# Kernel optimization log

Measured on AMD Instinct MI355X. Metric: run time of the kernel, lower is better.

## Reference

```python
import jax, jax.numpy as jnp
import numpy as np

WIDTH = 1.0  # radial_width
AMPLITUDE = (WIDTH ** 0.5) * 1.772637204826652  # ~sqrt(pi*width)
BN_EPS = 1e-3  # keras BatchNormalization default


def sine_pos_encoding(seq_len, hidden, dtype):
    # keras_nlp.layers.SinePositionEncoding, max_wavelength=10000
    position = jnp.arange(seq_len, dtype=dtype)
    min_freq = jnp.asarray(1.0 / 10000.0, dtype)
    timescales = min_freq ** (2 * (jnp.arange(hidden) // 2).astype(dtype) / hidden)
    angles = position[:, None] * timescales[None, :]  # [T, H]
    odd = (jnp.arange(hidden) % 2).astype(dtype)
    return jnp.sin(angles) * (1 - odd) + jnp.cos(angles) * odd


def setup_inputs() -> dict:
    key = jax.random.key(0)
    ks = jax.random.split(key, 4)
    B, T, C, F, K, L = 16, 4096, 8, 64, 11, 4096
    x = jax.random.normal(ks[0], (B, T, C), jnp.float32)
    conv_w = jax.random.normal(ks[1], (K, C, F), jnp.float32) * 0.1
    conv_b = jnp.zeros((F,), jnp.float32)
    gamma = jnp.ones((F,), jnp.float32)
    beta = jnp.zeros((F,), jnp.float32)
    mean = jnp.zeros((F,), jnp.float32)
    var = jnp.ones((F,), jnp.float32)
    # HeNormal init for dense
    dense_w = jax.random.normal(ks[2], (F, L), jnp.float32) * (2.0 / F) ** 0.5
    dense_b = jnp.zeros((L,), jnp.float32)
    return dict(x=x, conv_w=conv_w, conv_b=conv_b, gamma=gamma, beta=beta,
                mean=mean, var=var, dense_w=dense_w, dense_b=dense_b)


def reference(x, conv_w, conv_b, gamma, beta, mean, var, dense_w, dense_b):
    B, T, C = x.shape
    F = conv_w.shape[-1]
    L = dense_w.shape[-1]
    # Conv1D same padding -> [B, T, F]
    h = jax.lax.conv_general_dilated(x, conv_w, (1,), 'SAME',
                                     dimension_numbers=('NWC', 'WIO', 'NWC')) + conv_b
    # BatchNorm (inference form)
    h = (h - mean) / jnp.sqrt(var + BN_EPS) * gamma + beta
    # Softmax over time axis
    h = jax.nn.softmax(h, axis=1)
    # sine positional encoding added
    h = h + sine_pos_encoding(T, F, x.dtype)
    # Dense with sigmoid, rescale to [-1, 1]
    d = jax.nn.sigmoid(h @ dense_w + dense_b) * 2.0 - 1.0  # [B, T, L]
    # ReductionLayer: sum over time -> shift weights [B, L]
    shift = jnp.sum(d, axis=1)
    # ShiftingLayer: Gaussian RBF warp matrix then matmul
    idx_in = jnp.arange(1, T + 1, dtype=x.dtype)                       # [T]
    scale = jnp.asarray(T / L, x.dtype)
    idx_sh = (jnp.arange(1, L + 1, dtype=x.dtype) + shift) * scale     # [B, L]
    M = idx_in[None, None, :] - idx_sh[:, :, None]                     # [B, L, T]
    M = jnp.exp(-(M * M) / WIDTH) / AMPLITUDE
    return jnp.matmul(M, x)  # [B, L, C]
```

## Files before the change

kernel.cpp:

```cpp
#include <hip/hip_runtime.h>
#include <stdint.h>

#define BB 16
#define TT 4096
#define CC 8
#define FF 64
#define KW 11
#define LL 4096

#define L2E 1.442695040888963f
#define NCONV (BB * (TT / 64))

typedef __attribute__((ext_vector_type(8))) short short8;
typedef __attribute__((ext_vector_type(16))) float floatx16;

__device__ float e_buf[(size_t)BB * TT * FF];

__device__ __forceinline__ unsigned short f2b(float f) {
    union { float f; uint32_t i; } v; v.f = f;
    uint32_t x = v.i;
    return (unsigned short)((x + 0x7fffu + ((x >> 16) & 1u)) >> 16);
}
__device__ __forceinline__ float b2f(unsigned short u) {
    union { uint32_t i; float f; } v; v.i = ((uint32_t)u) << 16; return v.f;
}

#define DOT8(acc, ra, rb, wp) \
    acc = fmaf(ra.x, (wp)[0], acc); acc = fmaf(ra.y, (wp)[1], acc); \
    acc = fmaf(ra.z, (wp)[2], acc); acc = fmaf(ra.w, (wp)[3], acc); \
    acc = fmaf(rb.x, (wp)[4], acc); acc = fmaf(rb.y, (wp)[5], acc); \
    acc = fmaf(rb.z, (wp)[6], acc); acc = fmaf(rb.w, (wp)[7], acc);

__global__ __launch_bounds__(256) void k_convsplit(
        const float* __restrict__ x, const float* __restrict__ cw,
        const float* __restrict__ cb, const float* __restrict__ gm,
        const float* __restrict__ bt, const float* __restrict__ mn,
        const float* __restrict__ vr, const float* __restrict__ dw,
        unsigned short* __restrict__ Wt, float* __restrict__ sumexp) {
    if (blockIdx.x >= NCONV) {
        const int idx  = (blockIdx.x - NCONV) * 256 + threadIdx.x;
        const int j    = idx & 7;
        const int ln   = (idx >> 3) & 31;
        const int half = (idx >> 8) & 1;
        const int kf   = (idx >> 9) & 3;
        const int lt   = idx >> 11;
        const int l = lt * 32 + ln;
        const int k = kf * 16 + half * 8 + j;
        const float v = dw[(size_t)k * LL + l];
        const unsigned short hi = f2b(v);
        const unsigned short lo = f2b(v - b2f(hi));
        Wt[idx] = hi;
        Wt[262144 + idx] = lo;
        return;
    }
    __shared__ __align__(16) float xsm[(64 + KW - 1) * CC];
    __shared__ float red[4 * FF];
    const int tid = threadIdx.x;
    const int b  = blockIdx.x / (TT / 64);
    const int t0 = (blockIdx.x % (TT / 64)) * 64;
    const int f = tid & 63, ts = tid >> 6;

    float wreg[KW * CC];
#pragma unroll
    for (int kc = 0; kc < KW * CC; ++kc) wreg[kc] = cw[kc * FF + f];

    for (int i = tid; i < (64 + KW - 1) * CC; i += 256) {
        int row = i >> 3, c = i & 7;
        int t = t0 - (KW / 2) + row;
        xsm[i] = (t >= 0 && t < TT) ? x[((size_t)b * TT + t) * CC + c] : 0.0f;
    }
    const float s  = gm[f] * rsqrtf(vr[f] + 1e-3f);
    const float bb = bt[f] + (cb[f] - mn[f]) * s;
    const float s2 = s * L2E, b2 = bb * L2E;
    __syncthreads();

    float* eb = e_buf + ((size_t)b * TT + t0) * FF + f;
    const float4* xv = (const float4*)xsm;
    float esum = 0.f;
#pragma unroll 1
    for (int c = 0; c < 4; ++c) {
        const int tb = c * 16 + ts * 4;
        float a0 = 0.f, a1 = 0.f, a2 = 0.f, a3 = 0.f;
#pragma unroll
        for (int k = 0; k < KW + 3; ++k) {
            const float4 ra = xv[(tb + k) * 2];
            const float4 rb = xv[(tb + k) * 2 + 1];
            if (k <= 10)           { DOT8(a0, ra, rb, wreg + k * 8); }
            if (k >= 1 && k <= 11) { DOT8(a1, ra, rb, wreg + (k - 1) * 8); }
            if (k >= 2 && k <= 12) { DOT8(a2, ra, rb, wreg + (k - 2) * 8); }
            if (k >= 3)            { DOT8(a3, ra, rb, wreg + (k - 3) * 8); }
        }
        float e0 = __builtin_amdgcn_exp2f(fmaf(a0, s2, b2));
        float e1 = __builtin_amdgcn_exp2f(fmaf(a1, s2, b2));
        float e2 = __builtin_amdgcn_exp2f(fmaf(a2, s2, b2));
        float e3 = __builtin_amdgcn_exp2f(fmaf(a3, s2, b2));
        eb[(tb + 0) * FF] = e0;
        eb[(tb + 1) * FF] = e1;
        eb[(tb + 2) * FF] = e2;
        eb[(tb + 3) * FF] = e3;
        esum += (e0 + e1) + (e2 + e3);
    }
    red[ts * FF + f] = esum;
    __syncthreads();
    if (ts == 0) {
        float tot = red[f] + red[FF + f] + red[2 * FF + f] + red[3 * FF + f];
        atomicAdd(&sumexp[b * FF + f], tot);
    }
}

__global__ __launch_bounds__(512) void k_main(
        const unsigned short* __restrict__ Wt,
        const float* __restrict__ db,  const float* __restrict__ sumexp,
        float* __restrict__ shiftsum) {
    __shared__ __align__(16) unsigned short As[16384];

    const int tid = threadIdx.x;
    const int b  = blockIdx.y;
    const int t0 = blockIdx.x * 128;
    const int f = tid & 63, tq = tid >> 6;

    const float inv_se = 1.0f / sumexp[b * FF + f];
    const float tsf = exp2f(-0.20762050586796017f * (float)(f & ~1));
    const int kfh = ((f >> 4) << 1) | ((f >> 3) & 1);
    const int jj  = f & 7;
    const float ang0 = (float)(t0 + tq) * tsf;
    const float dA = 8.0f * tsf;
    float sv = sinf(ang0), cv = cosf(ang0);
    const float sd = sinf(dA), cd = cosf(dA);

    const float* eb = e_buf + ((size_t)b * TT + t0) * FF + f;
#pragma unroll 4
    for (int i = 0; i < 16; ++i) {
        const int tt = tq + 8 * i;
        float ev = eb[tt * FF];
        float p = (f & 1) ? cv : sv;
        float h = fmaf(ev, inv_se, p);
        const unsigned short hi = f2b(h);
        const unsigned short lo = f2b(h - b2f(hi));
        const int off = ((tt >> 5) * 8 + kfh) * 256 + (tt & 31) * 8 + jj;
        As[off] = hi;
        As[8192 + off] = lo;
        float ns = fmaf(sv, cd, cv * sd);
        float nc = fmaf(cv, cd, -(sv * sd));
        sv = ns; cv = nc;
    }
    __syncthreads();

    const int lane = tid & 63;
    const int wv   = tid >> 6;
    const int half = lane >> 5;
    const int ln31 = lane & 31;
    const int vbase = (half << 9) | (ln31 << 4);
    const char* Ab = (const char*)As;
    const char* Wb = (const char*)Wt;

#pragma unroll 1
    for (int i = 0; i < 16; ++i) {
        const int lt = (i + 2 * wv) & 15;
        const int ltile = lt * 8 + wv;
        const int lbase = ltile * 32;
        const char* wp = Wb + ((size_t)ltile << 12) + vbase;
        short8 Whi[4], Wlo[4];
#pragma unroll
        for (int kf = 0; kf < 4; ++kf) {
            Whi[kf] = *reinterpret_cast<const short8*>(wp + kf * 1024);
            Wlo[kf] = *reinterpret_cast<const short8*>(wp + 524288 + kf * 1024);
        }
        const float dbn = db[lbase + ln31] * (-L2E);

        float ss[4] = {0.f, 0.f, 0.f, 0.f};
#pragma unroll 1
        for (int nt = 0; nt < 4; ++nt) {
            const char* ap = Ab + (nt << 12) + vbase;
            floatx16 acc1 = {0.f, 0.f, 0.f, 0.f, 0.f, 0.f, 0.f, 0.f,
                             0.f, 0.f, 0.f, 0.f, 0.f, 0.f, 0.f, 0.f};
            floatx16 acc2 = acc1;
            __builtin_amdgcn_s_setprio(1);
            {
                short8 Ahi = *reinterpret_cast<const short8*>(ap);
                short8 Alo = *reinterpret_cast<const short8*>(ap + 16384);
                acc1 = __builtin_amdgcn_mfma_f32_32x32x16_bf16(Ahi, Whi[0], acc1, 0, 0, 0);
                acc1 = __builtin_amdgcn_mfma_f32_32x32x16_bf16(Alo, Whi[0], acc1, 0, 0, 0);
                acc1 = __builtin_amdgcn_mfma_f32_32x32x16_bf16(Ahi, Wlo[0], acc1, 0, 0, 0);
                Ahi = *reinterpret_cast<const short8*>(ap + 2048);
                Alo = *reinterpret_cast<const short8*>(ap + 16384 + 2048);
                acc2 = __builtin_amdgcn_mfma_f32_32x32x16_bf16(Ahi, Whi[2], acc2, 0, 0, 0);
                acc2 = __builtin_amdgcn_mfma_f32_32x32x16_bf16(Alo, Whi[2], acc2, 0, 0, 0);
                acc2 = __builtin_amdgcn_mfma_f32_32x32x16_bf16(Ahi, Wlo[2], acc2, 0, 0, 0);
                Ahi = *reinterpret_cast<const short8*>(ap + 1024);
                Alo = *reinterpret_cast<const short8*>(ap + 16384 + 1024);
                acc1 = __builtin_amdgcn_mfma_f32_32x32x16_bf16(Ahi, Whi[1], acc1, 0, 0, 0);
                acc1 = __builtin_amdgcn_mfma_f32_32x32x16_bf16(Alo, Whi[1], acc1, 0, 0, 0);
                acc1 = __builtin_amdgcn_mfma_f32_32x32x16_bf16(Ahi, Wlo[1], acc1, 0, 0, 0);
                Ahi = *reinterpret_cast<const short8*>(ap + 3072);
                Alo = *reinterpret_cast<const short8*>(ap + 16384 + 3072);
                acc2 = __builtin_amdgcn_mfma_f32_32x32x16_bf16(Ahi, Whi[3], acc2, 0, 0, 0);
                acc2 = __builtin_amdgcn_mfma_f32_32x32x16_bf16(Alo, Whi[3], acc2, 0, 0, 0);
                acc2 = __builtin_amdgcn_mfma_f32_32x32x16_bf16(Ahi, Wlo[3], acc2, 0, 0, 0);
            }
            __builtin_amdgcn_s_setprio(0);
#pragma unroll
            for (int q = 0; q < 4; ++q) {
                float e0 = __builtin_amdgcn_exp2f(fmaf(acc1[4 * q + 0], -L2E,
                                                  fmaf(acc2[4 * q + 0], -L2E, dbn)));
                float e1 = __builtin_amdgcn_exp2f(fmaf(acc1[4 * q + 1], -L2E,
                                                  fmaf(acc2[4 * q + 1], -L2E, dbn)));
                float e2 = __builtin_amdgcn_exp2f(fmaf(acc1[4 * q + 2], -L2E,
                                                  fmaf(acc2[4 * q + 2], -L2E, dbn)));
                float e3 = __builtin_amdgcn_exp2f(fmaf(acc1[4 * q + 3], -L2E,
                                                  fmaf(acc2[4 * q + 3], -L2E, dbn)));
                float a0 = 1.f + e0, a1 = 1.f + e1, a2 = 1.f + e2, a3 = 1.f + e3;
                float p01 = a0 * a1, p23 = a2 * a3;
                float num = fmaf(a0 + a1, p23, (a2 + a3) * p01);
                ss[q] = fmaf(num, __builtin_amdgcn_rcpf(p01 * p23), ss[q]);
            }
        }
        float ssum = (ss[0] + ss[1]) + (ss[2] + ss[3]);
        ssum += __shfl_xor(ssum, 32);
        if (half == 0)
            atomicAdd(shiftsum + (size_t)b * LL + lbase + ln31, ssum);
    }
}

__global__ __launch_bounds__(256) void k_warp(
        const float* __restrict__ shiftsum, const float* __restrict__ x,
        float* __restrict__ out) {
    const int idx = blockIdx.x * 256 + threadIdx.x;
    const int l = idx & (LL - 1);
    const int b = idx >> 12;
    const float sh = fmaf(2.0f, shiftsum[idx], -(float)TT);
    const float scale = (float)TT / (float)LL;
    const float center = ((float)(l + 1) + sh) * scale;
    const float R = 7.0f;
    int tlo = (int)ceilf(center - 1.0f - R);
    int thi = (int)floorf(center - 1.0f + R);
    if (tlo < 0) tlo = 0;
    if (thi > TT - 1) thi = TT - 1;
    float acc[CC];
#pragma unroll
    for (int c = 0; c < CC; ++c) acc[c] = 0.f;
    const float inv_amp = (float)(1.0 / 1.772637204826652);
    for (int t = tlo; t <= thi; ++t) {
        float d = (float)(t + 1) - center;
        float w = __expf(-d * d) * inv_amp;
        const float4 x0 = *reinterpret_cast<const float4*>(x + ((size_t)b * TT + t) * CC);
        const float4 x1 = *reinterpret_cast<const float4*>(x + ((size_t)b * TT + t) * CC + 4);
        acc[0] = fmaf(w, x0.x, acc[0]);
        acc[1] = fmaf(w, x0.y, acc[1]);
        acc[2] = fmaf(w, x0.z, acc[2]);
        acc[3] = fmaf(w, x0.w, acc[3]);
        acc[4] = fmaf(w, x1.x, acc[4]);
        acc[5] = fmaf(w, x1.y, acc[5]);
        acc[6] = fmaf(w, x1.z, acc[6]);
        acc[7] = fmaf(w, x1.w, acc[7]);
    }
    float* o = out + (size_t)idx * CC;
    *reinterpret_cast<float4*>(o)     = make_float4(acc[0], acc[1], acc[2], acc[3]);
    *reinterpret_cast<float4*>(o + 4) = make_float4(acc[4], acc[5], acc[6], acc[7]);
}

extern "C" void kernel_launch(void* const* d_in, const int* in_sizes, int n_in,
                              void* d_out, int out_size, void* d_ws, size_t ws_size,
                              hipStream_t stream) {
    const float* x  = (const float*)d_in[0];
    const float* cw = (const float*)d_in[1];
    const float* cb = (const float*)d_in[2];
    const float* gm = (const float*)d_in[3];
    const float* bt = (const float*)d_in[4];
    const float* mn = (const float*)d_in[5];
    const float* vr = (const float*)d_in[6];
    const float* dw = (const float*)d_in[7];
    const float* db = (const float*)d_in[8];

    float* sumexp      = (float*)d_ws;
    float* shiftsum    = sumexp + BB * FF;
    unsigned short* Wt = (unsigned short*)(shiftsum + BB * LL);

    hipMemsetAsync(sumexp, 0, (size_t)(BB * FF + BB * LL) * sizeof(float), stream);

    k_convsplit<<<NCONV + (FF * LL) / 256, 256, 0, stream>>>(
        x, cw, cb, gm, bt, mn, vr, dw, Wt, sumexp);
    k_main<<<dim3(TT / 128, BB), 512, 0, stream>>>(Wt, db, sumexp, shiftsum);
    k_warp<<<(BB * LL) / 256, 256, 0, stream>>>(shiftsum, x, (float*)d_out);
}
```

Baseline: 210.4 us.

## Replace atomics and memset with partial-sum buffers; fold sigmoid scale into MFMA

Float atomics into sumexp and shiftsum are replaced by per-block partial buffers that the consumer kernels reduce, and the hipMemsetAsync is dropped. The dense weights are pre-scaled by -log2(e) and the accumulator is seeded with the scaled bias, so the exp2 takes the MFMA output directly. This also merges the two accumulators into one fully unrolled chain. The cost is serial MFMA dependencies, extra partial-buffer reads in k_main and k_warp, and a different float summation order.

New measurement: 190.3 us. 9.5% less time.

```diff
diff --git a/kernel.cpp b/kernel.cpp
--- a/kernel.cpp
+++ b/kernel.cpp
@@ -15,6 +15,8 @@
 typedef __attribute__((ext_vector_type(16))) float floatx16;
 
 __device__ float e_buf[(size_t)BB * TT * FF];
+__device__ float sumpart[NCONV * FF];
+__device__ float shift_part[(size_t)BB * 32 * LL];
 
 __device__ __forceinline__ unsigned short f2b(float f) {
     union { float f; uint32_t i; } v; v.f = f;
@@ -36,7 +38,7 @@
         const float* __restrict__ cb, const float* __restrict__ gm,
         const float* __restrict__ bt, const float* __restrict__ mn,
         const float* __restrict__ vr, const float* __restrict__ dw,
-        unsigned short* __restrict__ Wt, float* __restrict__ sumexp) {
+        unsigned short* __restrict__ Wt) {
     if (blockIdx.x >= NCONV) {
         const int idx  = (blockIdx.x - NCONV) * 256 + threadIdx.x;
         const int j    = idx & 7;
@@ -46,7 +48,7 @@
         const int lt   = idx >> 11;
         const int l = lt * 32 + ln;
         const int k = kf * 16 + half * 8 + j;
-        const float v = dw[(size_t)k * LL + l];
+        const float v = dw[(size_t)k * LL + l] * (-L2E);
         const unsigned short hi = f2b(v);
         const unsigned short lo = f2b(v - b2f(hi));
         Wt[idx] = hi;
@@ -102,16 +104,13 @@
     }
     red[ts * FF + f] = esum;
     __syncthreads();
-    if (ts == 0) {
-        float tot = red[f] + red[FF + f] + red[2 * FF + f] + red[3 * FF + f];
-        atomicAdd(&sumexp[b * FF + f], tot);
-    }
+    if (ts == 0)
+        sumpart[blockIdx.x * FF + f] = red[f] + red[FF + f] + red[2 * FF + f] + red[3 * FF + f];
 }
 
 __global__ __launch_bounds__(512) void k_main(
         const unsigned short* __restrict__ Wt,
-        const float* __restrict__ db,  const float* __restrict__ sumexp,
-        float* __restrict__ shiftsum) {
+        const float* __restrict__ db, float* __restrict__ dummy) {
     __shared__ __align__(16) unsigned short As[16384];
 
     const int tid = threadIdx.x;
@@ -119,7 +118,12 @@
     const int t0 = blockIdx.x * 128;
     const int f = tid & 63, tq = tid >> 6;
 
-    const float inv_se = 1.0f / sumexp[b * FF + f];
+    float se = 0.f;
+    const float* sp = sumpart + (size_t)b * 64 * FF + f;
+#pragma unroll 8
+    for (int j = 0; j < 64; ++j) se += sp[j * FF];
+    const float inv_se = 1.0f / se;
+
     const float tsf = exp2f(-0.20762050586796017f * (float)(f & ~1));
     const int kfh = ((f >> 4) << 1) | ((f >> 3) & 1);
     const int jj  = f & 7;
@@ -169,46 +173,28 @@
         const float dbn = db[lbase + ln31] * (-L2E);
 
         float ss[4] = {0.f, 0.f, 0.f, 0.f};
-#pragma unroll 1
+#pragma unroll
         for (int nt = 0; nt < 4; ++nt) {
-            const char* ap = Ab + (nt << 12) + vbase;
-            floatx16 acc1 = {0.f, 0.f, 0.f, 0.f, 0.f, 0.f, 0.f, 0.f,
-                             0.f, 0.f, 0.f, 0.f, 0.f, 0.f, 0.f, 0.f};
-            floatx16 acc2 = acc1;
+            floatx16 acc;
+#pragma unroll
+            for (int r = 0; r < 16; ++r) acc[r] = dbn;
             __builtin_amdgcn_s_setprio(1);
-            {
-                short8 Ahi = *reinterpret_cast<const short8*>(ap);
-                short8 Alo = *reinterpret_cast<const short8*>(ap + 16384);
-                acc1 = __builtin_amdgcn_mfma_f32_32x32x16_bf16(Ahi, Whi[0], acc1, 0, 0, 0);
-                acc1 = __builtin_amdgcn_mfma_f32_32x32x16_bf16(Alo, Whi[0], acc1, 0, 0, 0);
-                acc1 = __builtin_amdgcn_mfma_f32_32x32x16_bf16(Ahi, Wlo[0], acc1, 0, 0, 0);
-                Ahi = *reinterpret_cast<const short8*>(ap + 2048);
-                Alo = *reinterpret_cast<const short8*>(ap + 16384 + 2048);
-                acc2 = __builtin_amdgcn_mfma_f32_32x32x16_bf16(Ahi, Whi[2], acc2, 0, 0, 0);
-                acc2 = __builtin_amdgcn_mfma_f32_32x32x16_bf16(Alo, Whi[2], acc2, 0, 0, 0);
-                acc2 = __builtin_amdgcn_mfma_f32_32x32x16_bf16(Ahi, Wlo[2], acc2, 0, 0, 0);
-                Ahi = *reinterpret_cast<const short8*>(ap + 1024);
-                Alo = *reinterpret_cast<const short8*>(ap + 16384 + 1024);
-                acc1 = __builtin_amdgcn_mfma_f32_32x32x16_bf16(Ahi, Whi[1], acc1, 0, 0, 0);
-                acc1 = __builtin_amdgcn_mfma_f32_32x32x16_bf16(Alo, Whi[1], acc1, 0, 0, 0);
-                acc1 = __builtin_amdgcn_mfma_f32_32x32x16_bf16(Ahi, Wlo[1], acc1, 0, 0, 0);
-                Ahi = *reinterpret_cast<const short8*>(ap + 3072);
-                Alo = *reinterpret_cast<const short8*>(ap + 16384 + 3072);
-                acc2 = __builtin_amdgcn_mfma_f32_32x32x16_bf16(Ahi, Whi[3], acc2, 0, 0, 0);
-                acc2 = __builtin_amdgcn_mfma_f32_32x32x16_bf16(Alo, Whi[3], acc2, 0, 0, 0);
-                acc2 = __builtin_amdgcn_mfma_f32_32x32x16_bf16(Ahi, Wlo[3], acc2, 0, 0, 0);
+#pragma unroll
+            for (int kf = 0; kf < 4; ++kf) {
+                const int ao = (nt * 8 + kf * 2) << 9;
+                short8 Ahi = *reinterpret_cast<const short8*>(Ab + ao + vbase);
+                short8 Alo = *reinterpret_cast<const short8*>(Ab + 16384 + ao + vbase);
+                acc = __builtin_amdgcn_mfma_f32_32x32x16_bf16(Ahi, Whi[kf], acc, 0, 0, 0);
+                acc = __builtin_amdgcn_mfma_f32_32x32x16_bf16(Alo, Whi[kf], acc, 0, 0, 0);
+                acc = __builtin_amdgcn_mfma_f32_32x32x16_bf16(Ahi, Wlo[kf], acc, 0, 0, 0);
             }
             __builtin_amdgcn_s_setprio(0);
 #pragma unroll
             for (int q = 0; q < 4; ++q) {
-                float e0 = __builtin_amdgcn_exp2f(fmaf(acc1[4 * q + 0], -L2E,
-                                                  fmaf(acc2[4 * q + 0], -L2E, dbn)));
-                float e1 = __builtin_amdgcn_exp2f(fmaf(acc1[4 * q + 1], -L2E,
-                                                  fmaf(acc2[4 * q + 1], -L2E, dbn)));
-                float e2 = __builtin_amdgcn_exp2f(fmaf(acc1[4 * q + 2], -L2E,
-                                                  fmaf(acc2[4 * q + 2], -L2E, dbn)));
-                float e3 = __builtin_amdgcn_exp2f(fmaf(acc1[4 * q + 3], -L2E,
-                                                  fmaf(acc2[4 * q + 3], -L2E, dbn)));
+                float e0 = __builtin_amdgcn_exp2f(acc[4 * q + 0]);
+                float e1 = __builtin_amdgcn_exp2f(acc[4 * q + 1]);
+                float e2 = __builtin_amdgcn_exp2f(acc[4 * q + 2]);
+                float e3 = __builtin_amdgcn_exp2f(acc[4 * q + 3]);
                 float a0 = 1.f + e0, a1 = 1.f + e1, a2 = 1.f + e2, a3 = 1.f + e3;
                 float p01 = a0 * a1, p23 = a2 * a3;
                 float num = fmaf(a0 + a1, p23, (a2 + a3) * p01);
@@ -218,17 +204,20 @@
         float ssum = (ss[0] + ss[1]) + (ss[2] + ss[3]);
         ssum += __shfl_xor(ssum, 32);
         if (half == 0)
-            atomicAdd(shiftsum + (size_t)b * LL + lbase + ln31, ssum);
+            shift_part[((size_t)b * 32 + blockIdx.x) * LL + lbase + ln31] = ssum;
     }
 }
 
 __global__ __launch_bounds__(256) void k_warp(
-        const float* __restrict__ shiftsum, const float* __restrict__ x,
-        float* __restrict__ out) {
+        const float* __restrict__ x, float* __restrict__ out) {
     const int idx = blockIdx.x * 256 + threadIdx.x;
     const int l = idx & (LL - 1);
     const int b = idx >> 12;
-    const float sh = fmaf(2.0f, shiftsum[idx], -(float)TT);
+    float S = 0.f;
+    const float* sp = shift_part + (size_t)b * 32 * LL + l;
+#pragma unroll 8
+    for (int tt = 0; tt < 32; ++tt) S += sp[tt * LL];
+    const float sh = fmaf(2.0f, S, -(float)TT);
     const float scale = (float)TT / (float)LL;
     const float center = ((float)(l + 1) + sh) * scale;
     const float R = 7.0f;
@@ -272,14 +261,10 @@
     const float* dw = (const float*)d_in[7];
     const float* db = (const float*)d_in[8];
 
-    float* sumexp      = (float*)d_ws;
-    float* shiftsum    = sumexp + BB * FF;
-    unsigned short* Wt = (unsigned short*)(shiftsum + BB * LL);
-
-    hipMemsetAsync(sumexp, 0, (size_t)(BB * FF + BB * LL) * sizeof(float), stream);
+    unsigned short* Wt = (unsigned short*)d_ws;
 
     k_convsplit<<<NCONV + (FF * LL) / 256, 256, 0, stream>>>(
-        x, cw, cb, gm, bt, mn, vr, dw, Wt, sumexp);
-    k_main<<<dim3(TT / 128, BB), 512, 0, stream>>>(Wt, db, sumexp, shiftsum);
-    k_warp<<<(BB * LL) / 256, 256, 0, stream>>>(shiftsum, x, (float*)d_out);
-}
+        x, cw, cb, gm, bt, mn, vr, dw, Wt);
+    k_main<<<dim3(TT / 128, BB), 512, 0, stream>>>(Wt, db, nullptr);
+    k_warp<<<(BB * LL) / 256, 256, 0, stream>>>(x, (float*)d_out);
+}
```
